# Performance work log

Measured on AMD Instinct MI355X. Metric: run time of the kernel, lower is better.

The kernel has to match this reference:

```python
import jax, jax.numpy as jnp
import numpy as np

N_NODES = 100000
N_EDGES = 1600000
D_IN, D_HID, D_OUT = 64, 64, 32


def _glorot(key, shape):
    fan_in = shape[0]
    return jax.random.normal(key, shape, dtype=jnp.float32) / np.sqrt(fan_in)


def setup_inputs() -> dict:
    key = jax.random.key(0)
    ks = jax.random.split(key, 12)
    x = jax.random.normal(ks[0], (N_NODES, D_IN), dtype=jnp.float32)
    edge_index = jax.random.randint(ks[1], (2, N_EDGES), 0, N_NODES, dtype=jnp.int32)
    dims = [(D_IN, D_HID), (D_HID, D_HID), (D_HID, D_OUT)]
    params = {}
    for i, (din, dout) in enumerate(dims):
        params[f"Wl{i}"] = _glorot(ks[2 + 3 * i], (din, dout))
        params[f"Wr{i}"] = _glorot(ks[3 + 3 * i], (din, dout))
        params[f"b{i}"] = jnp.zeros((dout,), dtype=jnp.float32)
    return {"x": x, "edge_index": edge_index, **params}


def _sage_conv(h, src, dst, deg_inv, Wl, Wr, b):
    # mean-aggregate neighbor features: gather from src, scatter-sum to dst
    msg_sum = jax.ops.segment_sum(h[src], dst, num_segments=N_NODES)  # [N, F]
    mean = msg_sum * deg_inv[:, None]
    # lin_l(mean) + bias + lin_r(h)  (PyG SAGEConv: bias lives in lin_l)
    return mean @ Wl + b + h @ Wr


def reference(x, edge_index, Wl0, Wr0, b0, Wl1, Wr1, b1, Wl2, Wr2, b2):
    src, dst = edge_index[0], edge_index[1]
    deg = jax.ops.segment_sum(jnp.ones((N_EDGES,), x.dtype), dst, num_segments=N_NODES)
    deg_inv = 1.0 / jnp.maximum(deg, 1.0)  # mean with clamp for isolated nodes
    h = jax.nn.elu(_sage_conv(x, src, dst, deg_inv, Wl0, Wr0, b0))
    h = jax.nn.elu(_sage_conv(h, src, dst, deg_inv, Wl1, Wr1, b1))
    return _sage_conv(h, src, dst, deg_inv, Wl2, Wr2, b2)
```

## Files before the change

kernel.cpp:

```cpp
#include <hip/hip_runtime.h>
#include <cstdint>
#include <cstddef>


constexpr int SBW = 256;
constexpr int LOGSBW = 8;
constexpr int CAPS = 4608;
constexpr int CHK = 2048;

typedef __attribute__((ext_vector_type(8))) short s16x8;
typedef __attribute__((ext_vector_type(4))) float f32x4;
typedef __attribute__((ext_vector_type(2))) float f32x2;

__device__ inline unsigned short f2bf(float f) {
  unsigned u = __builtin_bit_cast(unsigned, f);
  u += 0x7FFFu + ((u >> 16) & 1u);
  return (unsigned short)(u >> 16);
}
__device__ inline float bf2f(unsigned short b) {
  unsigned u = ((unsigned)b) << 16;
  return __builtin_bit_cast(float, u);
}
__device__ inline unsigned char f2fp8(float f) {
  int p = __builtin_amdgcn_cvt_pk_fp8_f32(f, f, 0, false);
  return (unsigned char)(p & 0xFF);
}


__global__ __launch_bounds__(256) void bin_coarse(const int* __restrict__ src,
                                                  const int* __restrict__ dst,
                                                  int* __restrict__ bcur,
                                                  unsigned int* __restrict__ coarse,
                                                  int NSB, int E) {
  __shared__ int h[512];
  __shared__ unsigned ed[CHK];
  __shared__ short sb[CHK];
  const int tid = threadIdx.x;
  for (int i = tid; i < NSB; i += 256) h[i] = 0;
  __syncthreads();
  const int e0 = blockIdx.x * CHK;
  const int e1 = min(E, e0 + CHK);
  for (int e = e0 + tid; e < e1; e += 256) {
    int d = dst[e];
    int s = src[e];
    int b = d >> LOGSBW;
    ed[e - e0] = (unsigned)s | ((unsigned)(d & (SBW - 1)) << 17);
    sb[e - e0] = (short)b;
    atomicAdd(&h[b], 1);
  }
  __syncthreads();
  for (int i = tid; i < NSB; i += 256) {
    int c = h[i];
    h[i] = c ? (i * CAPS + atomicAdd(&bcur[i], c)) : 0;
  }
  __syncthreads();
  const int n = e1 - e0;
  for (int k = tid; k < n; k += 256) {
    int b = sb[k];
    int pos = atomicAdd(&h[b], 1);
    if (pos < (b + 1) * CAPS)
      coarse[pos] = ed[k];
  }
}


__global__ __launch_bounds__(256) void super_csr(const unsigned int* __restrict__ coarse,
                                                 const int* __restrict__ bcur,
                                                 int* __restrict__ rowstart,
                                                 int* __restrict__ degarr,
                                                 float* __restrict__ deg_inv,
                                                 int* __restrict__ colidx,
                                                 int N) {
  __shared__ int cnt[SBW];
  __shared__ int sc[SBW];
  __shared__ int cur[SBW];
  const int b = blockIdx.x;
  const int tid = threadIdx.x;
  cnt[tid] = 0;
  __syncthreads();
  const int ec = min(bcur[b], CAPS);
  const int base = b * CAPS;
  for (int e = tid; e < ec; e += 256)
    atomicAdd(&cnt[coarse[base + e] >> 17], 1);
  __syncthreads();
  int v = cnt[tid];
  sc[tid] = v;
  __syncthreads();
  for (int off = 1; off < SBW; off <<= 1) {
    int y = sc[tid];
    if (tid >= off) y += sc[tid - off];
    __syncthreads();
    sc[tid] = y;
    __syncthreads();
  }
  int ex = sc[tid] - v;
  cur[tid] = ex;
  int gn = b * SBW + tid;
  if (gn < N) {
    rowstart[gn] = base + ex;
    degarr[gn] = v;
    deg_inv[gn] = 1.0f / (float)(v > 1 ? v : 1);
  }
  __syncthreads();
  for (int e = tid; e < ec; e += 256) {
    unsigned p = coarse[base + e];
    int dl = (int)(p >> 17);
    int s = (int)(p & 0x1FFFFu);
    int l = atomicAdd(&cur[dl], 1);
    colidx[base + l] = s;
  }
}


__global__ __launch_bounds__(256) void stage_w(const float* __restrict__ Wl0,
                                               const float* __restrict__ Wr0,
                                               const float* __restrict__ Wl1,
                                               const float* __restrict__ Wr1,
                                               const float* __restrict__ Wl2,
                                               const float* __restrict__ Wr2,
                                               unsigned short* __restrict__ Wsw) {
  int g = blockIdx.x * 256 + threadIdx.x;
  if (g >= 10240) return;
  int s = g * 2;
  int layer, off;
  if (s < 8192)       { layer = 0; off = 0; }
  else if (s < 16384) { layer = 1; off = 8192; }
  else                { layer = 2; off = 16384; }
  int t = s - off;
  int D = (layer == 2) ? 32 : 64;
  int NTT = D / 16;
  int tt = t >> 10;
  int rem = t & 1023;
  int plane = rem >> 9;
  int rem2 = rem & 511;
  int lane = rem2 >> 3;
  int j = rem2 & 7;
  int q = lane >> 4, m = lane & 15;
  int k = plane * 32 + q * 8 + j;
  const float* W;
  int c;
  if (tt < NTT) {
    c = tt;
    W = (layer == 0) ? Wl0 : (layer == 1) ? Wl1 : Wl2;
  } else {
    c = tt - NTT;
    W = (layer == 0) ? Wr0 : (layer == 1) ? Wr1 : Wr2;
  }
  int col = c * 16 + m;
  unsigned lo = f2bf(W[k * D + col]);
  unsigned hi = f2bf(W[(k + 1) * D + col]);
  *(unsigned*)&Wsw[s] = lo | (hi << 16);
}


__global__ __launch_bounds__(256) void gemm0_mfma(const float* __restrict__ x,
                                                  const unsigned short* __restrict__ Wf,
                                                  const float* __restrict__ bias,
                                                  unsigned char* __restrict__ t_out,
                                                  float* __restrict__ r_out, int N) {
  constexpr int DOUT = 64;
  constexpr int NTT = 4;
  const int tid = threadIdx.x;
  const int wv = tid >> 6, lane = tid & 63;
  const int q = lane >> 4, m = lane & 15;
  const int row = blockIdx.x * 64 + wv * 16 + m;
  const int rowc = row < N ? row : N - 1;
  const float* xp = &x[(size_t)rowc * 64];
  float4 f0 = *(const float4*)&xp[q * 8];
  float4 f1 = *(const float4*)&xp[q * 8 + 4];
  float4 f2 = *(const float4*)&xp[32 + q * 8];
  float4 f3 = *(const float4*)&xp[32 + q * 8 + 4];
  s16x8 a0, a1;
  a0[0] = (short)f2bf(f0.x); a0[1] = (short)f2bf(f0.y);
  a0[2] = (short)f2bf(f0.z); a0[3] = (short)f2bf(f0.w);
  a0[4] = (short)f2bf(f1.x); a0[5] = (short)f2bf(f1.y);
  a0[6] = (short)f2bf(f1.z); a0[7] = (short)f2bf(f1.w);
  a1[0] = (short)f2bf(f2.x); a1[1] = (short)f2bf(f2.y);
  a1[2] = (short)f2bf(f2.z); a1[3] = (short)f2bf(f2.w);
  a1[4] = (short)f2bf(f3.x); a1[5] = (short)f2bf(f3.y);
  a1[6] = (short)f2bf(f3.z); a1[7] = (short)f2bf(f3.w);

  f32x4 acc[2 * NTT];
#pragma unroll
  for (int c = 0; c < 2 * NTT; ++c) acc[c] = (f32x4){0.f, 0.f, 0.f, 0.f};
#pragma unroll
  for (int c = 0; c < 2 * NTT; ++c) {
    s16x8 b0 = *(const s16x8*)&Wf[(c * 2 + 0) * 512 + lane * 8];
    s16x8 b1 = *(const s16x8*)&Wf[(c * 2 + 1) * 512 + lane * 8];
    acc[c] = __builtin_amdgcn_mfma_f32_16x16x32_bf16(a0, b0, acc[c], 0, 0, 0);
    acc[c] = __builtin_amdgcn_mfma_f32_16x16x32_bf16(a1, b1, acc[c], 0, 0, 0);
  }

  const int orow = blockIdx.x * 64 + wv * 16 + q * 4;
#pragma unroll
  for (int c = 0; c < NTT; ++c) {
#pragma unroll
    for (int i = 0; i < 4; ++i) {
      int r_ = orow + i;
      if (r_ < N) t_out[(size_t)r_ * DOUT + c * 16 + m] = f2fp8(acc[c][i]);
    }
  }
#pragma unroll
  for (int c = 0; c < NTT; ++c) {
    float bv = bias[c * 16 + m];
#pragma unroll
    for (int i = 0; i < 4; ++i) {
      int r_ = orow + i;
      if (r_ < N) r_out[(size_t)r_ * DOUT + c * 16 + m] = acc[NTT + c][i] + bv;
    }
  }
}


template <int DOUT, bool TFP8>
__global__ __launch_bounds__(256) void gemm_mfma(const unsigned short* __restrict__ Hm,
                                                 const unsigned short* __restrict__ Wf,
                                                 const float* __restrict__ bias,
                                                 void* __restrict__ t_out,
                                                 float* __restrict__ r_out, int N) {
  constexpr int NTT = DOUT / 16;
  const int tid = threadIdx.x;
  const int wv = tid >> 6, lane = tid & 63;
  const int q = lane >> 4, m = lane & 15;
  const int row = blockIdx.x * 64 + wv * 16 + m;
  const int rowc = row < N ? row : N - 1;
  const s16x8 a0 = *(const s16x8*)&Hm[(size_t)rowc * 64 + q * 8];
  const s16x8 a1 = *(const s16x8*)&Hm[(size_t)rowc * 64 + 32 + q * 8];

  f32x4 acc[2 * NTT];
#pragma unroll
  for (int c = 0; c < 2 * NTT; ++c) acc[c] = (f32x4){0.f, 0.f, 0.f, 0.f};
#pragma unroll
  for (int c = 0; c < 2 * NTT; ++c) {
    s16x8 b0 = *(const s16x8*)&Wf[(c * 2 + 0) * 512 + lane * 8];
    s16x8 b1 = *(const s16x8*)&Wf[(c * 2 + 1) * 512 + lane * 8];
    acc[c] = __builtin_amdgcn_mfma_f32_16x16x32_bf16(a0, b0, acc[c], 0, 0, 0);
    acc[c] = __builtin_amdgcn_mfma_f32_16x16x32_bf16(a1, b1, acc[c], 0, 0, 0);
  }

  const int orow = blockIdx.x * 64 + wv * 16 + q * 4;
#pragma unroll
  for (int c = 0; c < NTT; ++c) {
#pragma unroll
    for (int i = 0; i < 4; ++i) {
      int r_ = orow + i;
      if (r_ < N) {
        if (TFP8)
          ((unsigned char*)t_out)[(size_t)r_ * DOUT + c * 16 + m] = f2fp8(acc[c][i]);
        else
          ((unsigned short*)t_out)[(size_t)r_ * DOUT + c * 16 + m] = f2bf(acc[c][i]);
      }
    }
  }
#pragma unroll
  for (int c = 0; c < NTT; ++c) {
    float bv = bias[c * 16 + m];
#pragma unroll
    for (int i = 0; i < 4; ++i) {
      int r_ = orow + i;
      if (r_ < N) r_out[(size_t)r_ * DOUT + c * 16 + m] = acc[NTT + c][i] + bv;
    }
  }
}


__global__ __launch_bounds__(256) void gather_fp8(const uint2* __restrict__ t,
                                                  const float* __restrict__ r,
                                                  const float* __restrict__ deg_inv,
                                                  const int* __restrict__ rowstart,
                                                  const int* __restrict__ degarr,
                                                  const int* __restrict__ colidx,
                                                  unsigned short* __restrict__ Xout,
                                                  int N) {
  int node = blockIdx.x * 32 + (threadIdx.x >> 3);
  int lane = threadIdx.x & 7;
  if (node >= N) return;
  int b = rowstart[node];
  int e = b + degarr[node];
  float s[8];
#pragma unroll
  for (int k = 0; k < 8; ++k) s[k] = 0.f;
  int i = b;
  for (; i + 8 <= e; i += 8) {
    uint2 v[8];
#pragma unroll
    for (int j = 0; j < 8; ++j)
      v[j] = t[(size_t)colidx[i + j] * 8 + lane];
#pragma unroll
    for (int j = 0; j < 8; ++j) {
      f32x2 p0 = __builtin_amdgcn_cvt_pk_f32_fp8((int)v[j].x, false);
      f32x2 p1 = __builtin_amdgcn_cvt_pk_f32_fp8((int)v[j].x, true);
      f32x2 p2 = __builtin_amdgcn_cvt_pk_f32_fp8((int)v[j].y, false);
      f32x2 p3 = __builtin_amdgcn_cvt_pk_f32_fp8((int)v[j].y, true);
      s[0] += p0[0]; s[1] += p0[1]; s[2] += p1[0]; s[3] += p1[1];
      s[4] += p2[0]; s[5] += p2[1]; s[6] += p3[0]; s[7] += p3[1];
    }
  }
  for (; i < e; ++i) {
    uint2 v = t[(size_t)colidx[i] * 8 + lane];
    f32x2 p0 = __builtin_amdgcn_cvt_pk_f32_fp8((int)v.x, false);
    f32x2 p1 = __builtin_amdgcn_cvt_pk_f32_fp8((int)v.x, true);
    f32x2 p2 = __builtin_amdgcn_cvt_pk_f32_fp8((int)v.y, false);
    f32x2 p3 = __builtin_amdgcn_cvt_pk_f32_fp8((int)v.y, true);
    s[0] += p0[0]; s[1] += p0[1]; s[2] += p1[0]; s[3] += p1[1];
    s[4] += p2[0]; s[5] += p2[1]; s[6] += p3[0]; s[7] += p3[1];
  }
  float dv = deg_inv[node];
  const float* rp = &r[(size_t)node * 64 + lane * 8];
  float4 r0 = *(const float4*)&rp[0];
  float4 r1 = *(const float4*)&rp[4];
  float a[8];
  a[0] = s[0] * dv + r0.x; a[1] = s[1] * dv + r0.y;
  a[2] = s[2] * dv + r0.z; a[3] = s[3] * dv + r0.w;
  a[4] = s[4] * dv + r1.x; a[5] = s[5] * dv + r1.y;
  a[6] = s[6] * dv + r1.z; a[7] = s[7] * dv + r1.w;
  s16x8 hv;
#pragma unroll
  for (int k = 0; k < 8; ++k) {
    float ak = a[k] > 0.f ? a[k] : (expf(a[k]) - 1.f);
    hv[k] = (short)f2bf(ak);
  }
  *(s16x8*)&Xout[(size_t)node * 64 + lane * 8] = hv;
}


__global__ __launch_bounds__(256) void gather_out(const uint2* __restrict__ t,
                                                  const float* __restrict__ r,
                                                  const float* __restrict__ deg_inv,
                                                  const int* __restrict__ rowstart,
                                                  const int* __restrict__ degarr,
                                                  const int* __restrict__ colidx,
                                                  float* __restrict__ out, int N) {
  constexpr int L = 8;
  int node = blockIdx.x * 32 + threadIdx.x / L;
  int lane = threadIdx.x & (L - 1);
  if (node >= N) return;
  int b = rowstart[node];
  int e = b + degarr[node];
  float s0 = 0.f, s1 = 0.f, s2 = 0.f, s3 = 0.f;
  int i = b;
  for (; i + 8 <= e; i += 8) {
    uint2 v[8];
#pragma unroll
    for (int j = 0; j < 8; ++j)
      v[j] = t[(size_t)colidx[i + j] * L + lane];
#pragma unroll
    for (int j = 0; j < 8; ++j) {
      s0 += bf2f((unsigned short)(v[j].x & 0xFFFFu));
      s1 += bf2f((unsigned short)(v[j].x >> 16));
      s2 += bf2f((unsigned short)(v[j].y & 0xFFFFu));
      s3 += bf2f((unsigned short)(v[j].y >> 16));
    }
  }
  for (; i < e; ++i) {
    uint2 v = t[(size_t)colidx[i] * L + lane];
    s0 += bf2f((unsigned short)(v.x & 0xFFFFu));
    s1 += bf2f((unsigned short)(v.x >> 16));
    s2 += bf2f((unsigned short)(v.y & 0xFFFFu));
    s3 += bf2f((unsigned short)(v.y >> 16));
  }
  float dv = deg_inv[node];
  float4 rv = *(const float4*)&r[(size_t)node * 32 + 4 * lane];
  *(float4*)&out[(size_t)node * 32 + 4 * lane] =
      make_float4(s0 * dv + rv.x, s1 * dv + rv.y, s2 * dv + rv.z, s3 * dv + rv.w);
}


extern "C" void kernel_launch(void* const* d_in, const int* in_sizes, int n_in,
                              void* d_out, int out_size, void* d_ws, size_t ws_size,
                              hipStream_t stream) {
  const float* x   = (const float*)d_in[0];
  const int*   ei  = (const int*)d_in[1];
  const float* Wl0 = (const float*)d_in[2];
  const float* Wr0 = (const float*)d_in[3];
  const float* b0  = (const float*)d_in[4];
  const float* Wl1 = (const float*)d_in[5];
  const float* Wr1 = (const float*)d_in[6];
  const float* b1  = (const float*)d_in[7];
  const float* Wl2 = (const float*)d_in[8];
  const float* Wr2 = (const float*)d_in[9];
  const float* b2  = (const float*)d_in[10];
  float* out = (float*)d_out;

  const int N = in_sizes[0] / 64;
  const int E = in_sizes[1] / 2;
  const int* srcv = ei;
  const int* dstv = ei + E;
  const int NSB = (N + SBW - 1) >> LOGSBW;

  auto al = [](size_t v) { return (v + 255) & ~(size_t)255; };
  char* w = (char*)d_ws;
  size_t oBcur = 0;
  size_t oRow  = oBcur + al(4 * (size_t)NSB);
  size_t oDeg  = oRow + al(4 * (size_t)N);
  size_t oDinv = oDeg + al(4 * (size_t)N);
  size_t oWsw  = oDinv + al(4 * (size_t)N);
  size_t oBin  = oWsw + al(2 * 20480);
  size_t oCol  = oBin + al(4 * (size_t)NSB * CAPS);
  size_t oP8   = oCol + al(4 * (size_t)NSB * CAPS);
  size_t oP16  = oP8 + al((size_t)N * 64);
  size_t oX    = oP16 + al(2 * (size_t)N * 32);
  size_t oR    = oX + al(2 * (size_t)N * 64);

  int*            bcur     = (int*)(w + oBcur);
  int*            rowstart = (int*)(w + oRow);
  int*            degarr   = (int*)(w + oDeg);
  float*          deg_inv  = (float*)(w + oDinv);
  unsigned short* Wsw      = (unsigned short*)(w + oWsw);
  unsigned*       coarse   = (unsigned*)(w + oBin);
  int*            colidx   = (int*)(w + oCol);
  unsigned char*  P8       = (unsigned char*)(w + oP8);
  unsigned short* P16      = (unsigned short*)(w + oP16);
  unsigned short* X        = (unsigned short*)(w + oX);
  float*          R        = (float*)(w + oR);

  hipMemsetAsync(bcur, 0, (size_t)NSB * 4, stream);

  stage_w<<<40, 256, 0, stream>>>(Wl0, Wr0, Wl1, Wr1, Wl2, Wr2, Wsw);
  int bbl = (E + CHK - 1) / CHK;
  bin_coarse<<<bbl, 256, 0, stream>>>(srcv, dstv, bcur, coarse, NSB, E);
  super_csr<<<NSB, 256, 0, stream>>>(coarse, bcur, rowstart, degarr, deg_inv, colidx, N);

  int gb = (N + 63) / 64;
  int ggb = (N + 31) / 32;
  gemm0_mfma<<<gb, 256, 0, stream>>>(x, Wsw, b0, P8, R, N);
  gather_fp8<<<ggb, 256, 0, stream>>>((const uint2*)P8, R, deg_inv, rowstart,
                                      degarr, colidx, X, N);
  gemm_mfma<64, true><<<gb, 256, 0, stream>>>(X, Wsw + 8192, b1, P8, R, N);
  gather_fp8<<<ggb, 256, 0, stream>>>((const uint2*)P8, R, deg_inv, rowstart,
                                      degarr, colidx, X, N);
  gemm_mfma<32, false><<<gb, 256, 0, stream>>>(X, Wsw + 16384, b2, P16, R, N);
  gather_out<<<ggb, 256, 0, stream>>>((const uint2*)P16, R, deg_inv, rowstart,
                                      degarr, colidx, out, N);
}
```

Measured before the change: 266.5 us.

## Pad CSR rows to multiples of eight, store residual in bf16, fuse weight staging

```diff
diff --git a/kernel.cpp b/kernel.cpp
--- a/kernel.cpp
+++ b/kernel.cpp
@@ -6,6 +6,7 @@
 constexpr int SBW = 256;
 constexpr int LOGSBW = 8;
 constexpr int CAPS = 4608;
+constexpr int CAPSP = 5632;
 constexpr int CHK = 2048;
 
 typedef __attribute__((ext_vector_type(8))) short s16x8;
@@ -27,15 +28,57 @@
 }
 
 
-__global__ __launch_bounds__(256) void bin_coarse(const int* __restrict__ src,
-                                                  const int* __restrict__ dst,
-                                                  int* __restrict__ bcur,
-                                                  unsigned int* __restrict__ coarse,
-                                                  int NSB, int E) {
+__global__ __launch_bounds__(256) void bin_stage(const int* __restrict__ src,
+                                                 const int* __restrict__ dst,
+                                                 int* __restrict__ bcur,
+                                                 unsigned int* __restrict__ coarse,
+                                                 int NSB, int E,
+                                                 const float* __restrict__ Wl0,
+                                                 const float* __restrict__ Wr0,
+                                                 const float* __restrict__ Wl1,
+                                                 const float* __restrict__ Wr1,
+                                                 const float* __restrict__ Wl2,
+                                                 const float* __restrict__ Wr2,
+                                                 unsigned short* __restrict__ Wsw) {
   __shared__ int h[512];
   __shared__ unsigned ed[CHK];
   __shared__ short sb[CHK];
   const int tid = threadIdx.x;
+  const int bbl = (E + CHK - 1) / CHK;
+  if ((int)blockIdx.x >= bbl) {
+    int g = (blockIdx.x - bbl) * 256 + tid;
+    if (g >= 10240) return;
+    int s = g * 2;
+    int layer, off;
+    if (s < 8192)       { layer = 0; off = 0; }
+    else if (s < 16384) { layer = 1; off = 8192; }
+    else                { layer = 2; off = 16384; }
+    int t = s - off;
+    int D = (layer == 2) ? 32 : 64;
+    int NTT = D / 16;
+    int tt = t >> 10;
+    int rem = t & 1023;
+    int plane = rem >> 9;
+    int rem2 = rem & 511;
+    int lane = rem2 >> 3;
+    int j = rem2 & 7;
+    int q = lane >> 4, m = lane & 15;
+    int k = plane * 32 + q * 8 + j;
+    const float* W;
+    int c;
+    if (tt < NTT) {
+      c = tt;
+      W = (layer == 0) ? Wl0 : (layer == 1) ? Wl1 : Wl2;
+    } else {
+      c = tt - NTT;
+      W = (layer == 0) ? Wr0 : (layer == 1) ? Wr1 : Wr2;
+    }
+    int col = c * 16 + m;
+    unsigned lo = f2bf(W[k * D + col]);
+    unsigned hi = f2bf(W[(k + 1) * D + col]);
+    *(unsigned*)&Wsw[s] = lo | (hi << 16);
+    return;
+  }
   for (int i = tid; i < NSB; i += 256) h[i] = 0;
   __syncthreads();
   const int e0 = blockIdx.x * CHK;
@@ -79,12 +122,14 @@
   cnt[tid] = 0;
   __syncthreads();
   const int ec = min(bcur[b], CAPS);
-  const int base = b * CAPS;
+  const int baseC = b * CAPS;
+  const int baseP = b * CAPSP;
   for (int e = tid; e < ec; e += 256)
-    atomicAdd(&cnt[coarse[base + e] >> 17], 1);
+    atomicAdd(&cnt[coarse[baseC + e] >> 17], 1);
   __syncthreads();
   int v = cnt[tid];
-  sc[tid] = v;
+  int pc = (v + 7) & ~7;
+  sc[tid] = pc;
   __syncthreads();
   for (int off = 1; off < SBW; off <<= 1) {
     int y = sc[tid];
@@ -93,63 +138,26 @@
     sc[tid] = y;
     __syncthreads();
   }
-  int ex = sc[tid] - v;
-  cur[tid] = ex;
+  int pex = sc[tid] - pc;
+  cur[tid] = pex;
   int gn = b * SBW + tid;
   if (gn < N) {
-    rowstart[gn] = base + ex;
-    degarr[gn] = v;
+    rowstart[gn] = baseP + pex;
+    degarr[gn] = pc;
     deg_inv[gn] = 1.0f / (float)(v > 1 ? v : 1);
   }
   __syncthreads();
   for (int e = tid; e < ec; e += 256) {
-    unsigned p = coarse[base + e];
+    unsigned p = coarse[baseC + e];
     int dl = (int)(p >> 17);
     int s = (int)(p & 0x1FFFFu);
     int l = atomicAdd(&cur[dl], 1);
-    colidx[base + l] = s;
-  }
-}
-
-
-__global__ __launch_bounds__(256) void stage_w(const float* __restrict__ Wl0,
-                                               const float* __restrict__ Wr0,
-                                               const float* __restrict__ Wl1,
-                                               const float* __restrict__ Wr1,
-                                               const float* __restrict__ Wl2,
-                                               const float* __restrict__ Wr2,
-                                               unsigned short* __restrict__ Wsw) {
-  int g = blockIdx.x * 256 + threadIdx.x;
-  if (g >= 10240) return;
-  int s = g * 2;
-  int layer, off;
-  if (s < 8192)       { layer = 0; off = 0; }
-  else if (s < 16384) { layer = 1; off = 8192; }
-  else                { layer = 2; off = 16384; }
-  int t = s - off;
-  int D = (layer == 2) ? 32 : 64;
-  int NTT = D / 16;
-  int tt = t >> 10;
-  int rem = t & 1023;
-  int plane = rem >> 9;
-  int rem2 = rem & 511;
-  int lane = rem2 >> 3;
-  int j = rem2 & 7;
-  int q = lane >> 4, m = lane & 15;
-  int k = plane * 32 + q * 8 + j;
-  const float* W;
-  int c;
-  if (tt < NTT) {
-    c = tt;
-    W = (layer == 0) ? Wl0 : (layer == 1) ? Wl1 : Wl2;
-  } else {
-    c = tt - NTT;
-    W = (layer == 0) ? Wr0 : (layer == 1) ? Wr1 : Wr2;
-  }
-  int col = c * 16 + m;
-  unsigned lo = f2bf(W[k * D + col]);
-  unsigned hi = f2bf(W[(k + 1) * D + col]);
-  *(unsigned*)&Wsw[s] = lo | (hi << 16);
+    if (l < CAPSP)
+      colidx[baseP + l] = s;
+  }
+  int pe = pex + pc;
+  if (pe > CAPSP) pe = CAPSP;
+  for (int l = pex + v; l < pe; ++l) colidx[baseP + l] = N;
 }
 
 
@@ -157,10 +165,13 @@
                                                   const unsigned short* __restrict__ Wf,
                                                   const float* __restrict__ bias,
                                                   unsigned char* __restrict__ t_out,
-                                                  float* __restrict__ r_out, int N) {
+                                                  unsigned short* __restrict__ r_out,
+                                                  int N) {
   constexpr int DOUT = 64;
   constexpr int NTT = 4;
   const int tid = threadIdx.x;
+  if (blockIdx.x == 0 && tid < 16)
+    ((unsigned*)t_out)[(size_t)N * 16 + tid] = 0u;
   const int wv = tid >> 6, lane = tid & 63;
   const int q = lane >> 4, m = lane & 15;
   const int row = blockIdx.x * 64 + wv * 16 + m;
@@ -206,20 +217,23 @@
 #pragma unroll
     for (int i = 0; i < 4; ++i) {
       int r_ = orow + i;
-      if (r_ < N) r_out[(size_t)r_ * DOUT + c * 16 + m] = acc[NTT + c][i] + bv;
-    }
-  }
-}
-
-
-template <int DOUT, bool TFP8>
+      if (r_ < N) r_out[(size_t)r_ * DOUT + c * 16 + m] = f2bf(acc[NTT + c][i] + bv);
+    }
+  }
+}
+
+
+template <int DOUT, bool TFP8, bool RB16>
 __global__ __launch_bounds__(256) void gemm_mfma(const unsigned short* __restrict__ Hm,
                                                  const unsigned short* __restrict__ Wf,
                                                  const float* __restrict__ bias,
                                                  void* __restrict__ t_out,
-                                                 float* __restrict__ r_out, int N) {
+                                                 void* __restrict__ r_out, int N) {
   constexpr int NTT = DOUT / 16;
+  constexpr int ROWB = TFP8 ? DOUT : DOUT * 2;
   const int tid = threadIdx.x;
+  if (blockIdx.x == 0 && tid < ROWB / 4)
+    ((unsigned*)((char*)t_out + (size_t)N * ROWB))[tid] = 0u;
   const int wv = tid >> 6, lane = tid & 63;
   const int q = lane >> 4, m = lane & 15;
   const int row = blockIdx.x * 64 + wv * 16 + m;
@@ -258,14 +272,20 @@
 #pragma unroll
     for (int i = 0; i < 4; ++i) {
       int r_ = orow + i;
-      if (r_ < N) r_out[(size_t)r_ * DOUT + c * 16 + m] = acc[NTT + c][i] + bv;
+      if (r_ < N) {
+        if (RB16)
+          ((unsigned short*)r_out)[(size_t)r_ * DOUT + c * 16 + m] =
+              f2bf(acc[NTT + c][i] + bv);
+        else
+          ((float*)r_out)[(size_t)r_ * DOUT + c * 16 + m] = acc[NTT + c][i] + bv;
+      }
     }
   }
 }
 
 
 __global__ __launch_bounds__(256) void gather_fp8(const uint2* __restrict__ t,
-                                                  const float* __restrict__ r,
+                                                  const unsigned short* __restrict__ r,
                                                   const float* __restrict__ deg_inv,
                                                   const int* __restrict__ rowstart,
                                                   const int* __restrict__ degarr,
@@ -280,12 +300,18 @@
   float s[8];
 #pragma unroll
   for (int k = 0; k < 8; ++k) s[k] = 0.f;
-  int i = b;
-  for (; i + 8 <= e; i += 8) {
+  for (int i = b; i < e; i += 8) {
+    int4 c0 = *(const int4*)&colidx[i];
+    int4 c1 = *(const int4*)&colidx[i + 4];
     uint2 v[8];
-#pragma unroll
-    for (int j = 0; j < 8; ++j)
-      v[j] = t[(size_t)colidx[i + j] * 8 + lane];
+    v[0] = t[(size_t)c0.x * 8 + lane];
+    v[1] = t[(size_t)c0.y * 8 + lane];
+    v[2] = t[(size_t)c0.z * 8 + lane];
+    v[3] = t[(size_t)c0.w * 8 + lane];
+    v[4] = t[(size_t)c1.x * 8 + lane];
+    v[5] = t[(size_t)c1.y * 8 + lane];
+    v[6] = t[(size_t)c1.z * 8 + lane];
+    v[7] = t[(size_t)c1.w * 8 + lane];
 #pragma unroll
     for (int j = 0; j < 8; ++j) {
       f32x2 p0 = __builtin_amdgcn_cvt_pk_f32_fp8((int)v[j].x, false);
@@ -296,24 +322,11 @@
       s[4] += p2[0]; s[5] += p2[1]; s[6] += p3[0]; s[7] += p3[1];
     }
   }
-  for (; i < e; ++i) {
-    uint2 v = t[(size_t)colidx[i] * 8 + lane];
-    f32x2 p0 = __builtin_amdgcn_cvt_pk_f32_fp8((int)v.x, false);
-    f32x2 p1 = __builtin_amdgcn_cvt_pk_f32_fp8((int)v.x, true);
-    f32x2 p2 = __builtin_amdgcn_cvt_pk_f32_fp8((int)v.y, false);
-    f32x2 p3 = __builtin_amdgcn_cvt_pk_f32_fp8((int)v.y, true);
-    s[0] += p0[0]; s[1] += p0[1]; s[2] += p1[0]; s[3] += p1[1];
-    s[4] += p2[0]; s[5] += p2[1]; s[6] += p3[0]; s[7] += p3[1];
-  }
   float dv = deg_inv[node];
-  const float* rp = &r[(size_t)node * 64 + lane * 8];
-  float4 r0 = *(const float4*)&rp[0];
-  float4 r1 = *(const float4*)&rp[4];
+  const s16x8 rv = *(const s16x8*)&r[(size_t)node * 64 + lane * 8];
   float a[8];
-  a[0] = s[0] * dv + r0.x; a[1] = s[1] * dv + r0.y;
-  a[2] = s[2] * dv + r0.z; a[3] = s[3] * dv + r0.w;
-  a[4] = s[4] * dv + r1.x; a[5] = s[5] * dv + r1.y;
-  a[6] = s[6] * dv + r1.z; a[7] = s[7] * dv + r1.w;
+#pragma unroll
+  for (int k = 0; k < 8; ++k) a[k] = s[k] * dv + bf2f((unsigned short)rv[k]);
   s16x8 hv;
 #pragma unroll
   for (int k = 0; k < 8; ++k) {
@@ -338,12 +351,18 @@
   int b = rowstart[node];
   int e = b + degarr[node];
   float s0 = 0.f, s1 = 0.f, s2 = 0.f, s3 = 0.f;
-  int i = b;
-  for (; i + 8 <= e; i += 8) {
+  for (int i = b; i < e; i += 8) {
+    int4 c0 = *(const int4*)&colidx[i];
+    int4 c1 = *(const int4*)&colidx[i + 4];
     uint2 v[8];
-#pragma unroll
-    for (int j = 0; j < 8; ++j)
-      v[j] = t[(size_t)colidx[i + j] * L + lane];
+    v[0] = t[(size_t)c0.x * L + lane];
+    v[1] = t[(size_t)c0.y * L + lane];
+    v[2] = t[(size_t)c0.z * L + lane];
+    v[3] = t[(size_t)c0.w * L + lane];
+    v[4] = t[(size_t)c1.x * L + lane];
+    v[5] = t[(size_t)c1.y * L + lane];
+    v[6] = t[(size_t)c1.z * L + lane];
+    v[7] = t[(size_t)c1.w * L + lane];
 #pragma unroll
     for (int j = 0; j < 8; ++j) {
       s0 += bf2f((unsigned short)(v[j].x & 0xFFFFu));
@@ -351,13 +370,6 @@
       s2 += bf2f((unsigned short)(v[j].y & 0xFFFFu));
       s3 += bf2f((unsigned short)(v[j].y >> 16));
     }
-  }
-  for (; i < e; ++i) {
-    uint2 v = t[(size_t)colidx[i] * L + lane];
-    s0 += bf2f((unsigned short)(v.x & 0xFFFFu));
-    s1 += bf2f((unsigned short)(v.x >> 16));
-    s2 += bf2f((unsigned short)(v.y & 0xFFFFu));
-    s3 += bf2f((unsigned short)(v.y >> 16));
   }
   float dv = deg_inv[node];
   float4 rv = *(const float4*)&r[(size_t)node * 32 + 4 * lane];
@@ -397,9 +409,9 @@
   size_t oWsw  = oDinv + al(4 * (size_t)N);
   size_t oBin  = oWsw + al(2 * 20480);
   size_t oCol  = oBin + al(4 * (size_t)NSB * CAPS);
-  size_t oP8   = oCol + al(4 * (size_t)NSB * CAPS);
-  size_t oP16  = oP8 + al((size_t)N * 64);
-  size_t oX    = oP16 + al(2 * (size_t)N * 32);
+  size_t oP8   = oCol + al(4 * (size_t)NSB * CAPSP);
+  size_t oP16  = oP8 + al((size_t)(N + 1) * 64);
+  size_t oX    = oP16 + al((size_t)(N + 1) * 64);
   size_t oR    = oX + al(2 * (size_t)N * 64);
 
   int*            bcur     = (int*)(w + oBcur);
@@ -412,24 +424,25 @@
   unsigned char*  P8       = (unsigned char*)(w + oP8);
   unsigned short* P16      = (unsigned short*)(w + oP16);
   unsigned short* X        = (unsigned short*)(w + oX);
-  float*          R        = (float*)(w + oR);
+  unsigned short* Rb       = (unsigned short*)(w + oR);
+  float*          Rf       = (float*)(w + oR);
 
   hipMemsetAsync(bcur, 0, (size_t)NSB * 4, stream);
 
-  stage_w<<<40, 256, 0, stream>>>(Wl0, Wr0, Wl1, Wr1, Wl2, Wr2, Wsw);
   int bbl = (E + CHK - 1) / CHK;
-  bin_coarse<<<bbl, 256, 0, stream>>>(srcv, dstv, bcur, coarse, NSB, E);
+  bin_stage<<<bbl + 40, 256, 0, stream>>>(srcv, dstv, bcur, coarse, NSB, E,
+                                          Wl0, Wr0, Wl1, Wr1, Wl2, Wr2, Wsw);
   super_csr<<<NSB, 256, 0, stream>>>(coarse, bcur, rowstart, degarr, deg_inv, colidx, N);
 
   int gb = (N + 63) / 64;
   int ggb = (N + 31) / 32;
-  gemm0_mfma<<<gb, 256, 0, stream>>>(x, Wsw, b0, P8, R, N);
-  gather_fp8<<<ggb, 256, 0, stream>>>((const uint2*)P8, R, deg_inv, rowstart,
+  gemm0_mfma<<<gb, 256, 0, stream>>>(x, Wsw, b0, P8, Rb, N);
+  gather_fp8<<<ggb, 256, 0, stream>>>((const uint2*)P8, Rb, deg_inv, rowstart,
                                       degarr, colidx, X, N);
-  gemm_mfma<64, true><<<gb, 256, 0, stream>>>(X, Wsw + 8192, b1, P8, R, N);
-  gather_fp8<<<ggb, 256, 0, stream>>>((const uint2*)P8, R, deg_inv, rowstart,
+  gemm_mfma<64, true, true><<<gb, 256, 0, stream>>>(X, Wsw + 8192, b1, P8, Rb, N);
+  gather_fp8<<<ggb, 256, 0, stream>>>((const uint2*)P8, Rb, deg_inv, rowstart,
                                       degarr, colidx, X, N);
-  gemm_mfma<32, false><<<gb, 256, 0, stream>>>(X, Wsw + 16384, b2, P16, R, N);
-  gather_out<<<ggb, 256, 0, stream>>>((const uint2*)P16, R, deg_inv, rowstart,
+  gemm_mfma<32, false, false><<<gb, 256, 0, stream>>>(X, Wsw + 16384, b2, P16, Rf, N);
+  gather_out<<<ggb, 256, 0, stream>>>((const uint2*)P16, Rf, deg_inv, rowstart,
                                       degarr, colidx, out, N);
 }
```

Measured after the change: 254.6 us. 1.05x faster.
